# Performance work log

Measured on AMD Instinct MI355X. Metric: run time of the kernel, lower is better.

Reference implementation:

```python
import jax, jax.numpy as jnp
import numpy as np

D_MODEL = 1024
NUM_HEAD = 16
D_K = D_MODEL // NUM_HEAD
FFN_D = 4096
EPS = 1e-5


def _layernorm(x, gamma, beta):
    mu = jnp.mean(x, axis=-1, keepdims=True)
    var = jnp.mean(jnp.square(x - mu), axis=-1, keepdims=True)
    return (x - mu) * jax.lax.rsqrt(var + EPS) * gamma + beta


def setup_inputs() -> dict:
    key = jax.random.key(0)
    ks = jax.random.split(key, 16)
    s = 1.0 / np.sqrt(D_MODEL)
    sf = 1.0 / np.sqrt(FFN_D)
    # weights stored as [in, out] (transpose of torch nn.Linear.weight)
    return {
        "x": jax.random.normal(ks[0], (4, 2048, D_MODEL), dtype=jnp.float32),
        "wq": jax.random.uniform(ks[1], (D_MODEL, D_MODEL), jnp.float32, -s, s),
        "bq": jax.random.uniform(ks[2], (D_MODEL,), jnp.float32, -s, s),
        "wk": jax.random.uniform(ks[3], (D_MODEL, D_MODEL), jnp.float32, -s, s),
        "bk": jax.random.uniform(ks[4], (D_MODEL,), jnp.float32, -s, s),
        "wv": jax.random.uniform(ks[5], (D_MODEL, D_MODEL), jnp.float32, -s, s),
        "bv": jax.random.uniform(ks[6], (D_MODEL,), jnp.float32, -s, s),
        "wo": jax.random.uniform(ks[7], (D_MODEL, D_MODEL), jnp.float32, -s, s),
        "bo": jax.random.uniform(ks[8], (D_MODEL,), jnp.float32, -s, s),
        "w1": jax.random.uniform(ks[9], (D_MODEL, FFN_D), jnp.float32, -s, s),
        "b1": jax.random.uniform(ks[10], (FFN_D,), jnp.float32, -s, s),
        "w2": jax.random.uniform(ks[11], (FFN_D, D_MODEL), jnp.float32, -sf, sf),
        "b2": jax.random.uniform(ks[12], (D_MODEL,), jnp.float32, -sf, sf),
        "g1": jnp.ones((D_MODEL,), jnp.float32),
        "be1": jnp.zeros((D_MODEL,), jnp.float32),
        "g2": jnp.ones((D_MODEL,), jnp.float32),
        "be2": jnp.zeros((D_MODEL,), jnp.float32),
    }


def reference(x, wq, bq, wk, bk, wv, bv, wo, bo, w1, b1, w2, b2, g1, be1, g2, be2):
    B, S, _ = x.shape
    resid1 = x
    # project and split heads: [B, H, S, d_k]
    def heads(w, b):
        return (x @ w + b).reshape(B, S, NUM_HEAD, D_K).transpose(0, 2, 1, 3)
    q = heads(wq, bq)
    k = heads(wk, bk)
    v = heads(wv, bv)
    scores = jnp.einsum("bhsd,bhtd->bhst", q, k) / jnp.sqrt(jnp.float32(D_K))
    attn = jax.nn.softmax(scores, axis=-1)
    ctx = jnp.einsum("bhst,bhtd->bhsd", attn, v)
    ctx = ctx.transpose(0, 2, 1, 3).reshape(B, S, D_MODEL)
    attn_out = ctx @ wo + bo
    x1 = _layernorm(resid1 + attn_out, g1, be1)
    ffn = jax.nn.relu(x1 @ w1 + b1) @ w2 + b2
    return _layernorm(x1 + ffn, g2, be2)
```

## Files before the change

kernel.cpp:

```cpp
#include <hip/hip_runtime.h>

typedef unsigned short u16;
typedef __attribute__((ext_vector_type(8))) u16 u16x8;
typedef __attribute__((ext_vector_type(8))) __bf16 bf16x8;
typedef __attribute__((ext_vector_type(4))) float floatx4;

#define MFMA16(a, b, c) __builtin_amdgcn_mfma_f32_16x16x32_bf16( \
    __builtin_bit_cast(bf16x8, a), __builtin_bit_cast(bf16x8, b), c, 0, 0, 0)

#if __has_builtin(__builtin_amdgcn_exp2f)
#define EXP2(x) __builtin_amdgcn_exp2f(x)
#else
#define EXP2(x) exp2f(x)
#endif

__device__ __forceinline__ float bf2f(u16 h) {
  unsigned u = ((unsigned)h) << 16;
  float f;
  __builtin_memcpy(&f, &u, 4);
  return f;
}
__device__ __forceinline__ u16 f2bf(float f) {
  unsigned u;
  __builtin_memcpy(&u, &f, 4);
  u += 0x7fff + ((u >> 16) & 1);
  return (u16)(u >> 16);
}
__device__ __forceinline__ u16 f2bf_rtz(float f) {
  unsigned u;
  __builtin_memcpy(&u, &f, 4);
  return (u16)(u >> 16);
}

typedef __attribute__((address_space(1))) const unsigned int gas_u32;
typedef __attribute__((address_space(3))) unsigned int las_u32;

__device__ __forceinline__ void gld_lds16(const u16* g, u16* l) {
  __builtin_amdgcn_global_load_lds((gas_u32*)g, (las_u32*)l, 16, 0, 0);
}

__global__ __launch_bounds__(256) void transpose_k(const float* __restrict__ in,
                                                   u16* __restrict__ out, int R, int C) {
  __shared__ u16 tile[64][65];
  int c0 = blockIdx.x * 64, r0 = blockIdx.y * 64;
  int tc = threadIdx.x & 63, tr = threadIdx.x >> 6;
#pragma unroll
  for (int i = 0; i < 16; ++i)
    tile[tr + i * 4][tc] = f2bf(in[(size_t)(r0 + tr + i * 4) * C + c0 + tc]);
  __syncthreads();
#pragma unroll
  for (int i = 0; i < 16; ++i)
    out[(size_t)(c0 + tr + i * 4) * R + r0 + tc] = tile[tc][tr + i * 4];
}

__global__ __launch_bounds__(256) void convert_k(const float* __restrict__ in,
                                                 u16* __restrict__ out) {
  size_t idx = ((size_t)blockIdx.x * 256 + threadIdx.x) * 8;
  floatx4 f0 = *(const floatx4*)(in + idx);
  floatx4 f1 = *(const floatx4*)(in + idx + 4);
  u16x8 o;
#pragma unroll
  for (int e = 0; e < 4; ++e) o[e] = f2bf(f0[e]);
#pragma unroll
  for (int e = 0; e < 4; ++e) o[4 + e] = f2bf(f1[e]);
  *(u16x8*)(out + idx) = o;
}

template <bool C_F32, bool BIAS_ROW>
__global__ __launch_bounds__(256, 2) void gemm_bt(const u16* __restrict__ A,
                                                  const u16* __restrict__ BT,
                                                  const float* __restrict__ bias,
                                                  void* __restrict__ Cv, int M, int N, int K,
                                                  int relu) {
  __shared__ __align__(16) u16 As[128 * 32];
  __shared__ __align__(16) u16 Bs[128 * 32];
  const int tid = threadIdx.x, lane = tid & 63, wave = tid >> 6;
  const int quad = lane >> 4, l15 = lane & 15;
  const int wr = wave >> 1, wc = wave & 1;
  const int m0 = blockIdx.x * 128, n0 = blockIdx.y * 128;

  floatx4 acc[4][4] = {};

  for (int k0 = 0; k0 < K; k0 += 32) {
#pragma unroll
    for (int p = 0; p < 2; ++p) {
      int chunk = p * 256 + tid;
      int row = chunk >> 2, cc = chunk & 3;
      int ldsbase = (p * 256 + wave * 64) * 8;
      gld_lds16(A + (size_t)(m0 + row) * K + k0 + cc * 8, As + ldsbase);
      gld_lds16(BT + (size_t)(n0 + row) * K + k0 + cc * 8, Bs + ldsbase);
    }
    __syncthreads();
    u16x8 af[4], bfr[4];
#pragma unroll
    for (int i = 0; i < 4; ++i)
      af[i] = *(const u16x8*)(As + (wr * 64 + i * 16 + l15) * 32 + quad * 8);
#pragma unroll
    for (int j = 0; j < 4; ++j)
      bfr[j] = *(const u16x8*)(Bs + (wc * 64 + j * 16 + l15) * 32 + quad * 8);
#pragma unroll
    for (int i = 0; i < 4; ++i)
#pragma unroll
      for (int j = 0; j < 4; ++j) acc[i][j] = MFMA16(af[i], bfr[j], acc[i][j]);
    __syncthreads();
  }

#pragma unroll
  for (int j = 0; j < 4; ++j) {
    int col = n0 + wc * 64 + j * 16 + l15;
    float bv = BIAS_ROW ? 0.f : bias[col];
#pragma unroll
    for (int i = 0; i < 4; ++i) {
      int row = m0 + wr * 64 + i * 16 + quad * 4;
#pragma unroll
      for (int r = 0; r < 4; ++r) {
        float v = acc[i][j][r] + (BIAS_ROW ? bias[row + r] : bv);
        if (relu) v = fmaxf(v, 0.f);
        if (C_F32)
          ((float*)Cv)[(size_t)(row + r) * N + col] = v;
        else
          ((u16*)Cv)[(size_t)(row + r) * N + col] = f2bf(v);
      }
    }
  }
}

__global__ __launch_bounds__(256, 2) void attn_k(const u16* __restrict__ Q,
                                                 const u16* __restrict__ Km,
                                                 const u16* __restrict__ Vt,
                                                 u16* __restrict__ O) {
  __shared__ __align__(16) u16 Ps[256 * 72];
  __shared__ __align__(16) u16 Ks[2][64 * 64];
  __shared__ __align__(16) u16 Vs[2][64 * 64];
  const int tid = threadIdx.x, lane = tid & 63, wave = tid >> 6;
  const int quad = lane >> 4, l15 = lane & 15;
  const int b = blockIdx.z, h = blockIdx.y, q0 = blockIdx.x * 256;
  const size_t tokbase = (size_t)b * 2048;

#pragma unroll
  for (int p = 0; p < 8; ++p) {
    int chunk = p * 256 + tid, row = chunk >> 3, cc = chunk & 7;
    u16x8 qv = *(const u16x8*)(Q + (tokbase + q0 + row) * 1024 + h * 64 + cc * 8);
#pragma unroll
    for (int e = 0; e < 8; ++e) qv[e] = f2bf(bf2f(qv[e]) * 0.18033688011f);
    *(u16x8*)(Ps + row * 72 + cc * 8) = qv;
  }
  __syncthreads();
  u16x8 qa[4][2];
#pragma unroll
  for (int i = 0; i < 4; ++i)
#pragma unroll
    for (int ks = 0; ks < 2; ++ks)
      qa[i][ks] = *(const u16x8*)(Ps + (wave * 64 + i * 16 + l15) * 72 + ks * 32 + quad * 8);

  floatx4 o[4][4] = {};
  float lsum[4][4] = {};

  auto stage = [&](int it2, int buf) {
    int t0 = it2 * 64;
#pragma unroll
    for (int p = 0; p < 2; ++p) {
      int chunk = p * 256 + tid;
      int row = chunk >> 3, cc = chunk & 7;
      int gc = cc ^ (row & 7);
      int ldsoff = (p * 256 + wave * 64) * 8;
      gld_lds16(Km + (tokbase + t0 + row) * 1024 + h * 64 + gc * 8, &Ks[buf][ldsoff]);
      gld_lds16(Vt + ((size_t)(h * 64 + row)) * 8192 + tokbase + t0 + gc * 8, &Vs[buf][ldsoff]);
    }
  };

  stage(0, 0);

  for (int it = 0; it < 32; ++it) {
    const int cur = it & 1;
    __syncthreads();
    if (it + 1 < 32) stage(it + 1, cur ^ 1);

    floatx4 s[4][4] = {};
#pragma unroll
    for (int ks = 0; ks < 2; ++ks) {
      u16x8 kb[4];
#pragma unroll
      for (int j = 0; j < 4; ++j)
        kb[j] = *(const u16x8*)(&Ks[cur][(j * 16 + l15) * 64 + (((ks * 4 + quad) ^ (l15 & 7)) * 8)]);
      __builtin_amdgcn_s_setprio(1);
#pragma unroll
      for (int i = 0; i < 4; ++i)
#pragma unroll
        for (int j = 0; j < 4; ++j) s[i][j] = MFMA16(qa[i][ks], kb[j], s[i][j]);
      __builtin_amdgcn_s_setprio(0);
    }

#pragma unroll
    for (int i = 0; i < 4; ++i)
#pragma unroll
      for (int r = 0; r < 4; ++r) {
        int prow = wave * 64 + i * 16 + quad * 4 + r;
        float ls = 0.f;
#pragma unroll
        for (int j = 0; j < 4; ++j) {
          float p = EXP2(s[i][j][r]);
          ls += p;
          Ps[prow * 72 + j * 16 + l15] = f2bf_rtz(p);
        }
        lsum[i][r] += ls;
      }
    asm volatile("s_waitcnt lgkmcnt(0)\n\ts_barrier" ::: "memory");

#pragma unroll
    for (int ks = 0; ks < 2; ++ks) {
      u16x8 pa[4], vbf[4];
#pragma unroll
      for (int i = 0; i < 4; ++i)
        pa[i] = *(const u16x8*)(Ps + (wave * 64 + i * 16 + l15) * 72 + ks * 32 + quad * 8);
#pragma unroll
      for (int jd = 0; jd < 4; ++jd)
        vbf[jd] = *(const u16x8*)(&Vs[cur][(jd * 16 + l15) * 64 + (((ks * 4 + quad) ^ (l15 & 7)) * 8)]);
      __builtin_amdgcn_s_setprio(1);
#pragma unroll
      for (int i = 0; i < 4; ++i)
#pragma unroll
        for (int jd = 0; jd < 4; ++jd) o[i][jd] = MFMA16(pa[i], vbf[jd], o[i][jd]);
      __builtin_amdgcn_s_setprio(0);
    }
  }

#pragma unroll
  for (int i = 0; i < 4; ++i) {
    float inv[4];
#pragma unroll
    for (int r = 0; r < 4; ++r) {
      float v = lsum[i][r];
#pragma unroll
      for (int mk = 1; mk < 16; mk <<= 1) v += __shfl_xor(v, mk);
      inv[r] = 1.0f / fmaxf(v, 1e-30f);
    }
#pragma unroll
    for (int jd = 0; jd < 4; ++jd)
#pragma unroll
      for (int r = 0; r < 4; ++r) {
        float val = o[i][jd][r] * inv[r];
        size_t tok = tokbase + q0 + wave * 64 + i * 16 + quad * 4 + r;
        O[tok * 1024 + h * 64 + jd * 16 + l15] = f2bf(val);
      }
  }
}

template <bool A_F32, bool B_F32, bool OUT_F32>
__global__ __launch_bounds__(256) void ln_k(const void* __restrict__ Av,
                                            const void* __restrict__ Bv,
                                            const float* __restrict__ g,
                                            const float* __restrict__ be,
                                            void* __restrict__ outv) {
  const int lane = threadIdx.x & 63, wave = threadIdx.x >> 6;
  const size_t row = (size_t)blockIdx.x * 4 + wave;
  const size_t base = row * 1024 + lane * 16;
  float v[16];
  if (A_F32) {
    const float* a = (const float*)Av + base;
#pragma unroll
    for (int q = 0; q < 4; ++q) {
      floatx4 t = *(const floatx4*)(a + q * 4);
#pragma unroll
      for (int e = 0; e < 4; ++e) v[q * 4 + e] = t[e];
    }
  } else {
    const u16* a = (const u16*)Av + base;
    u16x8 a0 = *(const u16x8*)a, a1 = *(const u16x8*)(a + 8);
#pragma unroll
    for (int e = 0; e < 8; ++e) {
      v[e] = bf2f(a0[e]);
      v[e + 8] = bf2f(a1[e]);
    }
  }
  if (B_F32) {
    const float* bb = (const float*)Bv + base;
#pragma unroll
    for (int q = 0; q < 4; ++q) {
      floatx4 t = *(const floatx4*)(bb + q * 4);
#pragma unroll
      for (int e = 0; e < 4; ++e) v[q * 4 + e] += t[e];
    }
  } else {
    const u16* bb = (const u16*)Bv + base;
    u16x8 b0 = *(const u16x8*)bb, b1 = *(const u16x8*)(bb + 8);
#pragma unroll
    for (int e = 0; e < 8; ++e) {
      v[e] += bf2f(b0[e]);
      v[e + 8] += bf2f(b1[e]);
    }
  }
  float sum = 0.f, sq = 0.f;
#pragma unroll
  for (int e = 0; e < 16; ++e) {
    sum += v[e];
    sq += v[e] * v[e];
  }
#pragma unroll
  for (int mk = 1; mk < 64; mk <<= 1) {
    sum += __shfl_xor(sum, mk);
    sq += __shfl_xor(sq, mk);
  }
  float mu = sum * (1.f / 1024.f);
  float var = fmaxf(sq * (1.f / 1024.f) - mu * mu, 0.f);
  float rstd = rsqrtf(var + 1e-5f);
  if (OUT_F32) {
    float* o = (float*)outv + base;
#pragma unroll
    for (int q = 0; q < 4; ++q) {
      floatx4 t;
#pragma unroll
      for (int e = 0; e < 4; ++e) {
        int c = lane * 16 + q * 4 + e;
        t[e] = (v[q * 4 + e] - mu) * rstd * g[c] + be[c];
      }
      *(floatx4*)(o + q * 4) = t;
    }
  } else {
    u16x8 o0, o1;
#pragma unroll
    for (int e = 0; e < 8; ++e) {
      int c = lane * 16 + e;
      o0[e] = f2bf((v[e] - mu) * rstd * g[c] + be[c]);
      o1[e] = f2bf((v[e + 8] - mu) * rstd * g[c + 8] + be[c + 8]);
    }
    *(u16x8*)((u16*)outv + base) = o0;
    *(u16x8*)((u16*)outv + base + 8) = o1;
  }
}

extern "C" void kernel_launch(void* const* d_in, const int* in_sizes, int n_in, void* d_out,
                              int out_size, void* d_ws, size_t ws_size, hipStream_t stream) {
  const float* x = (const float*)d_in[0];
  const float* wq = (const float*)d_in[1];
  const float* bq = (const float*)d_in[2];
  const float* wk = (const float*)d_in[3];
  const float* bk = (const float*)d_in[4];
  const float* wv = (const float*)d_in[5];
  const float* bv = (const float*)d_in[6];
  const float* wo = (const float*)d_in[7];
  const float* bo = (const float*)d_in[8];
  const float* w1 = (const float*)d_in[9];
  const float* b1 = (const float*)d_in[10];
  const float* w2 = (const float*)d_in[11];
  const float* b2 = (const float*)d_in[12];
  const float* g1 = (const float*)d_in[13];
  const float* be1 = (const float*)d_in[14];
  const float* g2 = (const float*)d_in[15];
  const float* be2 = (const float*)d_in[16];
  float* out = (float*)d_out;

  u16* W = (u16*)d_ws;
  const size_t M1 = (size_t)1 << 20;
  u16* wqT = W;
  u16* wkT = wqT + M1;
  u16* wvT = wkT + M1;
  u16* woT = wvT + M1;
  u16* w1T = woT + M1;
  u16* w2T = w1T + 4 * M1;
  u16* arena = w2T + 4 * M1;
  const size_t S8M = (size_t)8 << 20;
  u16* xb = arena;
  u16* Qb = arena + S8M;
  u16* Kb = arena + 2 * S8M;
  u16* Vtb = arena + 3 * S8M;
  u16* Cb = arena + 4 * S8M;
  u16* AO = Qb;
  u16* X1 = xb;
  u16* F1 = Qb;

  dim3 blk(256);
  transpose_k<<<dim3(16, 16), blk, 0, stream>>>(wq, wqT, 1024, 1024);
  transpose_k<<<dim3(16, 16), blk, 0, stream>>>(wk, wkT, 1024, 1024);
  transpose_k<<<dim3(16, 16), blk, 0, stream>>>(wv, wvT, 1024, 1024);
  transpose_k<<<dim3(16, 16), blk, 0, stream>>>(wo, woT, 1024, 1024);
  transpose_k<<<dim3(64, 16), blk, 0, stream>>>(w1, w1T, 1024, 4096);
  transpose_k<<<dim3(16, 64), blk, 0, stream>>>(w2, w2T, 4096, 1024);
  convert_k<<<4096, blk, 0, stream>>>(x, xb);

  gemm_bt<false, false><<<dim3(64, 8), blk, 0, stream>>>(xb, wqT, bq, Qb, 8192, 1024, 1024, 0);
  gemm_bt<false, false><<<dim3(64, 8), blk, 0, stream>>>(xb, wkT, bk, Kb, 8192, 1024, 1024, 0);
  gemm_bt<false, true><<<dim3(8, 64), blk, 0, stream>>>(wvT, xb, bv, Vtb, 1024, 8192, 1024, 0);

  attn_k<<<dim3(8, 16, 4), blk, 0, stream>>>(Qb, Kb, Vtb, Cb);

  gemm_bt<false, false><<<dim3(64, 8), blk, 0, stream>>>(Cb, woT, bo, AO, 8192, 1024, 1024, 0);
  ln_k<true, false, false><<<2048, blk, 0, stream>>>(x, AO, g1, be1, X1);

  gemm_bt<false, false><<<dim3(64, 32), blk, 0, stream>>>(X1, w1T, b1, F1, 8192, 4096, 1024, 1);
  gemm_bt<true, false><<<dim3(64, 8), blk, 0, stream>>>(F1, w2T, b2, out, 8192, 1024, 4096, 0);
  ln_k<false, true, true><<<2048, blk, 0, stream>>>(X1, out, g2, be2, out);
}
```

Before: 561.5 us.

## Rewrite attention with 32x32 MFMA, register-resident P via permlane swap

The attention kernel now uses 32x32x16 bf16 MFMAs and computes S transposed (K as the A operand, Q as B). The exponentiated probabilities are packed with v_cvt_pk_bf16 and rearranged in registers with v_permlane32_swap, so they feed the PV MFMA directly without the LDS round trip and the mid-iteration barrier. Each block now handles 128 query rows, giving twice as many blocks and higher target occupancy (launch bounds 4). Output is staged through LDS for coalesced 16-byte stores, and Q is loaded via global_load_lds. The risks are the correctness of the permlane fragment layout and register pressure at the higher occupancy.

Result: slower. 575.7 us (+2.5%).

```diff
diff --git a/kernel.cpp b/kernel.cpp
--- a/kernel.cpp
+++ b/kernel.cpp
@@ -4,8 +4,12 @@
 typedef __attribute__((ext_vector_type(8))) u16 u16x8;
 typedef __attribute__((ext_vector_type(8))) __bf16 bf16x8;
 typedef __attribute__((ext_vector_type(4))) float floatx4;
+typedef __attribute__((ext_vector_type(16))) float floatx16;
+typedef __attribute__((ext_vector_type(4))) unsigned int u32x4;
 
 #define MFMA16(a, b, c) __builtin_amdgcn_mfma_f32_16x16x32_bf16( \
+    __builtin_bit_cast(bf16x8, a), __builtin_bit_cast(bf16x8, b), c, 0, 0, 0)
+#define MFMA32(a, b, c) __builtin_amdgcn_mfma_f32_32x32x16_bf16( \
     __builtin_bit_cast(bf16x8, a), __builtin_bit_cast(bf16x8, b), c, 0, 0, 0)
 
 #if __has_builtin(__builtin_amdgcn_exp2f)
@@ -26,10 +30,14 @@
   u += 0x7fff + ((u >> 16) & 1);
   return (u16)(u >> 16);
 }
-__device__ __forceinline__ u16 f2bf_rtz(float f) {
-  unsigned u;
-  __builtin_memcpy(&u, &f, 4);
-  return (u16)(u >> 16);
+
+__device__ __forceinline__ unsigned cvt_pk_bf16(float a, float b) {
+  unsigned r;
+  asm("v_cvt_pk_bf16_f32 %0, %1, %2" : "=v"(r) : "v"(a), "v"(b));
+  return r;
+}
+__device__ __forceinline__ void pl32_swap(unsigned& a, unsigned& b) {
+  asm("v_permlane32_swap_b32 %0, %1" : "+v"(a), "+v"(b));
 }
 
 typedef __attribute__((address_space(1))) const unsigned int gas_u32;
@@ -125,36 +133,37 @@
   }
 }
 
-__global__ __launch_bounds__(256, 2) void attn_k(const u16* __restrict__ Q,
+__global__ __launch_bounds__(256, 4) void attn_k(const u16* __restrict__ Q,
                                                  const u16* __restrict__ Km,
                                                  const u16* __restrict__ Vt,
                                                  u16* __restrict__ O) {
-  __shared__ __align__(16) u16 Ps[256 * 72];
-  __shared__ __align__(16) u16 Ks[2][64 * 64];
-  __shared__ __align__(16) u16 Vs[2][64 * 64];
-  const int tid = threadIdx.x, lane = tid & 63, wave = tid >> 6;
-  const int quad = lane >> 4, l15 = lane & 15;
-  const int b = blockIdx.z, h = blockIdx.y, q0 = blockIdx.x * 256;
+  __shared__ __align__(16) u16 sh[16384];
+  const int tid = threadIdx.x, lane = tid & 63, w = tid >> 6;
+  const int hi = lane >> 5, l31 = lane & 31;
+  const int b = blockIdx.z, h = blockIdx.y, q0 = blockIdx.x * 128;
   const size_t tokbase = (size_t)b * 2048;
 
 #pragma unroll
-  for (int p = 0; p < 8; ++p) {
+  for (int p = 0; p < 4; ++p) {
     int chunk = p * 256 + tid, row = chunk >> 3, cc = chunk & 7;
-    u16x8 qv = *(const u16x8*)(Q + (tokbase + q0 + row) * 1024 + h * 64 + cc * 8);
-#pragma unroll
-    for (int e = 0; e < 8; ++e) qv[e] = f2bf(bf2f(qv[e]) * 0.18033688011f);
-    *(u16x8*)(Ps + row * 72 + cc * 8) = qv;
+    int gc = cc ^ (row & 7);
+    gld_lds16(Q + (tokbase + q0 + row) * 1024 + h * 64 + gc * 8, sh + (p * 256 + w * 64) * 8);
   }
   __syncthreads();
-  u16x8 qa[4][2];
-#pragma unroll
-  for (int i = 0; i < 4; ++i)
-#pragma unroll
-    for (int ks = 0; ks < 2; ++ks)
-      qa[i][ks] = *(const u16x8*)(Ps + (wave * 64 + i * 16 + l15) * 72 + ks * 32 + quad * 8);
-
-  floatx4 o[4][4] = {};
-  float lsum[4][4] = {};
+  u16x8 qf[4];
+#pragma unroll
+  for (int kt = 0; kt < 4; ++kt) {
+    int r = w * 32 + l31;
+    int sel = (kt * 2 + hi) ^ (r & 7);
+    u16x8 t = *(const u16x8*)(sh + r * 64 + sel * 8);
+#pragma unroll
+    for (int e = 0; e < 8; ++e) t[e] = f2bf(bf2f(t[e]) * 0.18033688011f);
+    qf[kt] = t;
+  }
+  __syncthreads();
+
+  floatx16 oacc0 = {}, oacc1 = {};
+  float lsum = 0.f;
 
   auto stage = [&](int it2, int buf) {
     int t0 = it2 * 64;
@@ -163,9 +172,10 @@
       int chunk = p * 256 + tid;
       int row = chunk >> 3, cc = chunk & 7;
       int gc = cc ^ (row & 7);
-      int ldsoff = (p * 256 + wave * 64) * 8;
-      gld_lds16(Km + (tokbase + t0 + row) * 1024 + h * 64 + gc * 8, &Ks[buf][ldsoff]);
-      gld_lds16(Vt + ((size_t)(h * 64 + row)) * 8192 + tokbase + t0 + gc * 8, &Vs[buf][ldsoff]);
+      int ldsoff = (p * 256 + w * 64) * 8;
+      gld_lds16(Km + (tokbase + t0 + row) * 1024 + h * 64 + gc * 8, sh + buf * 4096 + ldsoff);
+      gld_lds16(Vt + ((size_t)(h * 64 + row)) * 8192 + tokbase + t0 + gc * 8,
+                sh + 8192 + buf * 4096 + ldsoff);
     }
   };
 
@@ -175,74 +185,89 @@
     const int cur = it & 1;
     __syncthreads();
     if (it + 1 < 32) stage(it + 1, cur ^ 1);
-
-    floatx4 s[4][4] = {};
-#pragma unroll
-    for (int ks = 0; ks < 2; ++ks) {
-      u16x8 kb[4];
-#pragma unroll
-      for (int j = 0; j < 4; ++j)
-        kb[j] = *(const u16x8*)(&Ks[cur][(j * 16 + l15) * 64 + (((ks * 4 + quad) ^ (l15 & 7)) * 8)]);
+    const u16* kb = sh + cur * 4096;
+    const u16* vb = sh + 8192 + cur * 4096;
+
+    u32x4 pf[4];
+#pragma unroll
+    for (int tt = 0; tt < 2; ++tt) {
+      u16x8 ka[4];
+#pragma unroll
+      for (int kt = 0; kt < 4; ++kt) {
+        int r = tt * 32 + l31;
+        ka[kt] = *(const u16x8*)(kb + r * 64 + (((kt * 2 + hi) ^ (r & 7)) * 8));
+      }
+      floatx16 s = {};
       __builtin_amdgcn_s_setprio(1);
 #pragma unroll
-      for (int i = 0; i < 4; ++i)
-#pragma unroll
-        for (int j = 0; j < 4; ++j) s[i][j] = MFMA16(qa[i][ks], kb[j], s[i][j]);
+      for (int kt = 0; kt < 4; ++kt) s = MFMA32(ka[kt], qf[kt], s);
       __builtin_amdgcn_s_setprio(0);
-    }
-
-#pragma unroll
-    for (int i = 0; i < 4; ++i)
-#pragma unroll
-      for (int r = 0; r < 4; ++r) {
-        int prow = wave * 64 + i * 16 + quad * 4 + r;
-        float ls = 0.f;
-#pragma unroll
-        for (int j = 0; j < 4; ++j) {
-          float p = EXP2(s[i][j][r]);
-          ls += p;
-          Ps[prow * 72 + j * 16 + l15] = f2bf_rtz(p);
-        }
-        lsum[i][r] += ls;
-      }
-    asm volatile("s_waitcnt lgkmcnt(0)\n\ts_barrier" ::: "memory");
-
-#pragma unroll
-    for (int ks = 0; ks < 2; ++ks) {
-      u16x8 pa[4], vbf[4];
-#pragma unroll
-      for (int i = 0; i < 4; ++i)
-        pa[i] = *(const u16x8*)(Ps + (wave * 64 + i * 16 + l15) * 72 + ks * 32 + quad * 8);
-#pragma unroll
-      for (int jd = 0; jd < 4; ++jd)
-        vbf[jd] = *(const u16x8*)(&Vs[cur][(jd * 16 + l15) * 64 + (((ks * 4 + quad) ^ (l15 & 7)) * 8)]);
+
+      float p[16];
+#pragma unroll
+      for (int r = 0; r < 16; ++r) p[r] = EXP2(s[r]);
+#pragma unroll
+      for (int r = 0; r < 16; ++r) lsum += p[r];
+#pragma unroll
+      for (int half = 0; half < 2; ++half) {
+        unsigned X0 = cvt_pk_bf16(p[half * 8 + 0], p[half * 8 + 1]);
+        unsigned X1 = cvt_pk_bf16(p[half * 8 + 2], p[half * 8 + 3]);
+        unsigned Y0 = cvt_pk_bf16(p[half * 8 + 4], p[half * 8 + 5]);
+        unsigned Y1 = cvt_pk_bf16(p[half * 8 + 6], p[half * 8 + 7]);
+        pl32_swap(X0, Y0);
+        pl32_swap(X1, Y1);
+        u32x4 f;
+        f[0] = X0; f[1] = X1; f[2] = Y0; f[3] = Y1;
+        pf[tt * 2 + half] = f;
+      }
+    }
+
+    {
+      u16x8 va[4];
+#pragma unroll
+      for (int kt = 0; kt < 4; ++kt) {
+        int r = l31;
+        va[kt] = *(const u16x8*)(vb + r * 64 + (((kt * 2 + hi) ^ (r & 7)) * 8));
+      }
       __builtin_amdgcn_s_setprio(1);
 #pragma unroll
-      for (int i = 0; i < 4; ++i)
-#pragma unroll
-        for (int jd = 0; jd < 4; ++jd) o[i][jd] = MFMA16(pa[i], vbf[jd], o[i][jd]);
+      for (int kt = 0; kt < 4; ++kt)
+        oacc0 = MFMA32(va[kt], __builtin_bit_cast(u16x8, pf[kt]), oacc0);
       __builtin_amdgcn_s_setprio(0);
-    }
-  }
-
-#pragma unroll
-  for (int i = 0; i < 4; ++i) {
-    float inv[4];
-#pragma unroll
-    for (int r = 0; r < 4; ++r) {
-      float v = lsum[i][r];
-#pragma unroll
-      for (int mk = 1; mk < 16; mk <<= 1) v += __shfl_xor(v, mk);
-      inv[r] = 1.0f / fmaxf(v, 1e-30f);
-    }
-#pragma unroll
-    for (int jd = 0; jd < 4; ++jd)
-#pragma unroll
-      for (int r = 0; r < 4; ++r) {
-        float val = o[i][jd][r] * inv[r];
-        size_t tok = tokbase + q0 + wave * 64 + i * 16 + quad * 4 + r;
-        O[tok * 1024 + h * 64 + jd * 16 + l15] = f2bf(val);
-      }
+#pragma unroll
+      for (int kt = 0; kt < 4; ++kt) {
+        int r = 32 + l31;
+        va[kt] = *(const u16x8*)(vb + r * 64 + (((kt * 2 + hi) ^ (r & 7)) * 8));
+      }
+      __builtin_amdgcn_s_setprio(1);
+#pragma unroll
+      for (int kt = 0; kt < 4; ++kt)
+        oacc1 = MFMA32(va[kt], __builtin_bit_cast(u16x8, pf[kt]), oacc1);
+      __builtin_amdgcn_s_setprio(0);
+    }
+  }
+
+  __syncthreads();
+  float tot = lsum + __shfl_xor(lsum, 32);
+  float inv = 1.0f / fmaxf(tot, 1e-30f);
+  const int qrow = w * 32 + l31;
+#pragma unroll
+  for (int dt = 0; dt < 2; ++dt) {
+    const floatx16& oa = dt ? oacc1 : oacc0;
+#pragma unroll
+    for (int pr = 0; pr < 8; ++pr) {
+      float a = oa[2 * pr] * inv, bb = oa[2 * pr + 1] * inv;
+      unsigned pkw = (unsigned)f2bf(a) | ((unsigned)f2bf(bb) << 16);
+      int d = dt * 32 + (pr & 1) * 2 + (pr >> 1) * 8 + 4 * hi;
+      *(unsigned*)(sh + qrow * 72 + d) = pkw;
+    }
+  }
+  __syncthreads();
+#pragma unroll
+  for (int p2 = 0; p2 < 4; ++p2) {
+    int c = p2 * 64 + lane, rl = c >> 3, cc = c & 7;
+    u16x8 vv = *(const u16x8*)(sh + (w * 32 + rl) * 72 + cc * 8);
+    *(u16x8*)(O + (tokbase + q0 + w * 32 + rl) * 1024 + h * 64 + cc * 8) = vv;
   }
 }
 
@@ -382,7 +407,7 @@
   gemm_bt<false, false><<<dim3(64, 8), blk, 0, stream>>>(xb, wkT, bk, Kb, 8192, 1024, 1024, 0);
   gemm_bt<false, true><<<dim3(8, 64), blk, 0, stream>>>(wvT, xb, bv, Vtb, 1024, 8192, 1024, 0);
 
-  attn_k<<<dim3(8, 16, 4), blk, 0, stream>>>(Qb, Kb, Vtb, Cb);
+  attn_k<<<dim3(16, 16, 4), blk, 0, stream>>>(Qb, Kb, Vtb, Cb);
 
   gemm_bt<false, false><<<dim3(64, 8), blk, 0, stream>>>(Cb, woT, bo, AO, 8192, 1024, 1024, 0);
   ln_k<true, false, false><<<2048, blk, 0, stream>>>(x, AO, g1, be1, X1);
```
